# Performance work log

Hardware: AMD Instinct MI355X
Metric: run time of the kernel (lower is better)

The kernel has to match this reference:

```python
import jax, jax.numpy as jnp
import numpy as np


def setup_inputs() -> dict:
    key = jax.random.key(0)
    ks = jax.random.split(key, 12)
    T, A, B = 1024, 32, 8
    V, D = 100000, 128
    H1, H2, C = 512, 256, 100
    s = 0.05
    return {
        "diag_idx": jax.random.randint(ks[0], (T, A, B), 0, V),
        "proc_idx": jax.random.randint(ks[1], (T, A, B), 0, V),
        "embedding": jax.random.normal(ks[2], (V, D), jnp.float32) * s,
        "W_ih": jax.random.normal(ks[3], (4 * H1, 2 * D), jnp.float32) * s,
        "W_hh": jax.random.normal(ks[4], (4 * H1, H1), jnp.float32) * s,
        "b_ih": jax.random.normal(ks[5], (4 * H1,), jnp.float32) * s,
        "b_hh": jax.random.normal(ks[6], (4 * H1,), jnp.float32) * s,
        "W1": jax.random.normal(ks[7], (H2, H1), jnp.float32) * s,
        "b1": jax.random.normal(ks[8], (H2,), jnp.float32) * s,
        "W_out": jax.random.normal(ks[9], (C, H2), jnp.float32) * s,
        "b_out": jax.random.normal(ks[10], (C,), jnp.float32) * s,
    }


def _pool(embedding, idx):
    # idx: [T, A, B] -> gather [T, A, B, D]; mean over items (B), sum over sets (A)
    e = embedding[idx]
    return e.mean(axis=2).sum(axis=1)  # [T, D]


def _lstm(x, W_ih, W_hh, b_ih, b_hh):
    # x: [T, 2D]; PyTorch gate order: i, f, g, o
    H = W_hh.shape[1]
    gx = x @ W_ih.T + (b_ih + b_hh)  # [T, 4H]

    def step(carry, gx_t):
        h, c = carry
        gates = gx_t + h @ W_hh.T
        i, f, g, o = jnp.split(gates, 4)
        i, f, o = jax.nn.sigmoid(i), jax.nn.sigmoid(f), jax.nn.sigmoid(o)
        g = jnp.tanh(g)
        c = f * c + i * g
        h = o * jnp.tanh(c)
        return (h, c), h

    h0 = jnp.zeros((H,), x.dtype)
    c0 = jnp.zeros((H,), x.dtype)
    _, hs = jax.lax.scan(step, (h0, c0), gx)
    return hs  # [T, H]


def reference(diag_idx, proc_idx, embedding, W_ih, W_hh, b_ih, b_hh, W1, b1, W_out, b_out):
    d_vec = _pool(embedding, diag_idx)   # [T, D]
    p_vec = _pool(embedding, proc_idx)   # [T, D]
    x = jnp.concatenate([d_vec, p_vec], axis=-1)  # [T, 2D]
    hs = _lstm(x, W_ih, W_hh, b_ih, b_hh)         # [T, H1]
    h1 = jax.nn.relu(hs @ W1.T + b1)              # [T, H2]
    return h1 @ W_out.T + b_out                   # [T, n_class]
```

## Files before the change

kernel.cpp:

```cpp
#include <hip/hip_runtime.h>

#define T_STEPS 1024
#define A_SETS 32
#define B_ITEMS 8
#define D_EMB 128
#define H1 512
#define H2 256
#define NCLS 100
#define G4H 2048
#define X_DIM 256

#define OFF_X    0
#define OFF_GX   (OFF_X + T_STEPS * X_DIM)
#define OFF_HS   (OFF_GX + T_STEPS * G4H)
#define OFF_SLOT (OFF_HS + T_STEPS * H1)

#define LSTM_G 16

__global__ void init_kernel(float* __restrict__ ws) {
    int tid = threadIdx.x;
    ws[OFF_SLOT + tid] = 0.f;
    ws[OFF_SLOT + 1024 + tid] = 0.f;
}

__global__ void pool_kernel(const int* __restrict__ diag, const int* __restrict__ proc,
                            const float* __restrict__ emb, float* __restrict__ ws) {
    __shared__ int sidx[2][A_SETS * B_ITEMS];
    int t = blockIdx.x;
    int tid = threadIdx.x;
    sidx[0][tid] = diag[t * 256 + tid];
    sidx[1][tid] = proc[t * 256 + tid];
    __syncthreads();
    int src = tid >> 7;
    int d = tid & 127;
    float acc = 0.f;
#pragma unroll 8
    for (int i = 0; i < 256; ++i) {
        acc += emb[(size_t)sidx[src][i] * D_EMB + d];
    }
    ws[OFF_X + t * X_DIM + src * D_EMB + d] = acc * 0.125f;
}

#define GX_TB 8
__global__ void gx_kernel(const float* __restrict__ W_ih, const float* __restrict__ b_ih,
                          const float* __restrict__ b_hh, float* __restrict__ ws) {
    __shared__ float xs[GX_TB][X_DIM];
    int tb = blockIdx.x;
    int jb = blockIdx.y;
    int tid = threadIdx.x;
    const float* x = ws + OFF_X;
    for (int i = tid; i < GX_TB * X_DIM; i += 256)
        xs[i >> 8][i & 255] = x[(size_t)(tb * GX_TB + (i >> 8)) * X_DIM + (i & 255)];
    __syncthreads();
    int row = jb * 256 + tid;
    float b = b_ih[row] + b_hh[row];
    float acc[GX_TB];
#pragma unroll
    for (int i = 0; i < GX_TB; ++i) acc[i] = b;
    const float4* wr = (const float4*)(W_ih + (size_t)row * X_DIM);
#pragma unroll 4
    for (int k4 = 0; k4 < X_DIM / 4; ++k4) {
        float4 w = wr[k4];
#pragma unroll
        for (int i = 0; i < GX_TB; ++i) {
            acc[i] = fmaf(w.x, xs[i][4 * k4 + 0], acc[i]);
            acc[i] = fmaf(w.y, xs[i][4 * k4 + 1], acc[i]);
            acc[i] = fmaf(w.z, xs[i][4 * k4 + 2], acc[i]);
            acc[i] = fmaf(w.w, xs[i][4 * k4 + 3], acc[i]);
        }
    }
    float* gx = ws + OFF_GX;
#pragma unroll
    for (int i = 0; i < GX_TB; ++i)
        gx[(size_t)(tb * GX_TB + i) * G4H + row] = acc[i];
}

__global__ void __launch_bounds__(512, 1)
lstm_kernel(const float* __restrict__ W_hh, float* __restrict__ ws) {
    __shared__ float h_pad[2][4 * 136];
    const int g = blockIdx.x;
    const int tid = threadIdx.x;
    const int lane = tid & 63;
    const int j = tid >> 4;
    const int seg = (tid >> 2) & 3;
    const int gate = tid & 3;
    const int unit = g * 32 + j;
    const int grow = gate * H1 + unit;

    float w[128];
    {
        const float4* wr = (const float4*)(W_hh + (size_t)grow * H1 + seg * 128);
#pragma unroll
        for (int k = 0; k < 32; ++k) {
            float4 v = wr[k];
            w[4 * k + 0] = v.x; w[4 * k + 1] = v.y;
            w[4 * k + 2] = v.z; w[4 * k + 3] = v.w;
        }
    }

    unsigned long long* slots = (unsigned long long*)(ws + OFF_SLOT);
    float* hs = ws + OFF_HS;
    const float* gx = ws + OFF_GX;
    const int stage_row = tid >> 7;
    const int stage_col = tid & 127;
    const bool comb = ((tid & 15) == 0);
    const int base = lane & 48;
    float c = 0.f;

    for (int s = 1; s <= T_STEPS; ++s) {
        const int t = s - 1;
        float gxv = gx[(size_t)t * G4H + grow];
        const unsigned need = (unsigned)(s - 1);
        unsigned long long v;
        do {
            v = __hip_atomic_load(&slots[((s - 1) & 1) * H1 + tid],
                                  __ATOMIC_RELAXED, __HIP_MEMORY_SCOPE_AGENT);
        } while ((unsigned)(v >> 32) < need);
        float* hp = h_pad[s & 1];
        hp[stage_row * 136 + stage_col] = __uint_as_float((unsigned)v);
        __syncthreads();
        float acc = 0.f;
        const float4* h4 = (const float4*)(hp + seg * 136);
#pragma unroll
        for (int k = 0; k < 32; ++k) {
            float4 hv = h4[k];
            acc = fmaf(w[4 * k + 0], hv.x, acc);
            acc = fmaf(w[4 * k + 1], hv.y, acc);
            acc = fmaf(w[4 * k + 2], hv.z, acc);
            acc = fmaf(w[4 * k + 3], hv.w, acc);
        }
        acc += __shfl_xor(acc, 4);
        acc += __shfl_xor(acc, 8);
        acc += gxv;
        float gi = __shfl(acc, base + 0);
        float gf = __shfl(acc, base + 1);
        float gg = __shfl(acc, base + 2);
        float go = __shfl(acc, base + 3);
        if (comb) {
            gi = 1.f / (1.f + __expf(-gi));
            gf = 1.f / (1.f + __expf(-gf));
            go = 1.f / (1.f + __expf(-go));
            gg = tanhf(gg);
            c = fmaf(gf, c, gi * gg);
            float h = go * tanhf(c);
            unsigned long long pv =
                ((unsigned long long)(unsigned)s << 32) | (unsigned long long)__float_as_uint(h);
            __hip_atomic_store(&slots[(s & 1) * H1 + unit], pv,
                               __ATOMIC_RELAXED, __HIP_MEMORY_SCOPE_AGENT);
            hs[(size_t)t * H1 + unit] = h;
        }
    }
}

__global__ void mlp_kernel(const float* __restrict__ W1, const float* __restrict__ b1,
                           const float* __restrict__ W_out, const float* __restrict__ b_out,
                           const float* __restrict__ ws, float* __restrict__ out) {
    __shared__ float hsv[H1];
    __shared__ float h1v[H2];
    int t = blockIdx.x;
    int tid = threadIdx.x;
    const float* hs = ws + OFF_HS;
    hsv[tid] = hs[(size_t)t * H1 + tid];
    hsv[256 + tid] = hs[(size_t)t * H1 + 256 + tid];
    __syncthreads();
    float acc = b1[tid];
    const float4* wr = (const float4*)(W1 + (size_t)tid * H1);
#pragma unroll 4
    for (int k = 0; k < H1 / 4; ++k) {
        float4 w = wr[k];
        acc = fmaf(w.x, hsv[4 * k + 0], acc);
        acc = fmaf(w.y, hsv[4 * k + 1], acc);
        acc = fmaf(w.z, hsv[4 * k + 2], acc);
        acc = fmaf(w.w, hsv[4 * k + 3], acc);
    }
    h1v[tid] = fmaxf(acc, 0.f);
    __syncthreads();
    if (tid < NCLS) {
        float a2 = b_out[tid];
        const float4* w2 = (const float4*)(W_out + (size_t)tid * H2);
#pragma unroll 4
        for (int k = 0; k < H2 / 4; ++k) {
            float4 w = w2[k];
            a2 = fmaf(w.x, h1v[4 * k + 0], a2);
            a2 = fmaf(w.y, h1v[4 * k + 1], a2);
            a2 = fmaf(w.z, h1v[4 * k + 2], a2);
            a2 = fmaf(w.w, h1v[4 * k + 3], a2);
        }
        out[(size_t)t * NCLS + tid] = a2;
    }
}

extern "C" void kernel_launch(void* const* d_in, const int* in_sizes, int n_in,
                              void* d_out, int out_size, void* d_ws, size_t ws_size,
                              hipStream_t stream) {
    const int* diag = (const int*)d_in[0];
    const int* proc = (const int*)d_in[1];
    const float* emb = (const float*)d_in[2];
    const float* W_ih = (const float*)d_in[3];
    const float* W_hh = (const float*)d_in[4];
    const float* b_ih = (const float*)d_in[5];
    const float* b_hh = (const float*)d_in[6];
    const float* W1 = (const float*)d_in[7];
    const float* b1 = (const float*)d_in[8];
    const float* W_out = (const float*)d_in[9];
    const float* b_out = (const float*)d_in[10];
    float* ws = (float*)d_ws;
    float* out = (float*)d_out;

    hipLaunchKernelGGL(init_kernel, dim3(1), dim3(1024), 0, stream, ws);
    hipLaunchKernelGGL(pool_kernel, dim3(T_STEPS), dim3(256), 0, stream, diag, proc, emb, ws);
    hipLaunchKernelGGL(gx_kernel, dim3(T_STEPS / GX_TB, G4H / 256), dim3(256), 0, stream,
                       W_ih, b_ih, b_hh, ws);
    hipLaunchKernelGGL(lstm_kernel, dim3(LSTM_G), dim3(512), 0, stream, W_hh, ws);
    hipLaunchKernelGGL(mlp_kernel, dim3(T_STEPS), dim3(256), 0, stream,
                       W1, b1, W_out, b_out, ws, out);
}
```

Measured before the change: 2.870 ms.

## Spread LSTM recurrence over 32 blocks, use fast gate math, batch MLP timesteps

The persistent LSTM kernel now runs on 32 blocks with 16 hidden units each. Each thread holds 64 weights instead of 128, which cuts per-step FMA chain length and register pressure, at the cost of an extra shuffle reduction and more blocks joining the global spin-wait handshake. The sigmoid and tanh are rewritten with exp plus a hardware reciprocal refined by one Newton step, shortening the serial per-step critical path with slightly different rounding. The MLP kernel processes 8 timesteps per block, so each W1/W_out row load is reused across them, with fewer blocks in exchange.

```diff
diff --git a/kernel.cpp b/kernel.cpp
--- a/kernel.cpp
+++ b/kernel.cpp
@@ -15,7 +15,18 @@
 #define OFF_HS   (OFF_GX + T_STEPS * G4H)
 #define OFF_SLOT (OFF_HS + T_STEPS * H1)
 
-#define LSTM_G 16
+#define LSTM_G 32
+
+__device__ __forceinline__ float fast_rcp(float d) {
+    float r = __builtin_amdgcn_rcpf(d);
+    return r * (2.f - d * r);
+}
+__device__ __forceinline__ float fast_sigmoid(float x) {
+    return fast_rcp(1.f + __expf(-x));
+}
+__device__ __forceinline__ float fast_tanh(float x) {
+    return 1.f - 2.f * fast_rcp(1.f + __expf(2.f * x));
+}
 
 __global__ void init_kernel(float* __restrict__ ws) {
     int tid = threadIdx.x;
@@ -75,36 +86,31 @@
         gx[(size_t)(tb * GX_TB + i) * G4H + row] = acc[i];
 }
 
-__global__ void __launch_bounds__(512, 1)
+__global__ void __launch_bounds__(512, 2)
 lstm_kernel(const float* __restrict__ W_hh, float* __restrict__ ws) {
-    __shared__ float h_pad[2][4 * 136];
+    __shared__ float h_pad[2][8 * 68];
     const int g = blockIdx.x;
     const int tid = threadIdx.x;
     const int lane = tid & 63;
-    const int j = tid >> 4;
-    const int seg = (tid >> 2) & 3;
+    const int j = tid >> 5;
+    const int seg = (tid >> 2) & 7;
     const int gate = tid & 3;
-    const int unit = g * 32 + j;
+    const int unit = g * 16 + j;
     const int grow = gate * H1 + unit;
 
-    float w[128];
+    float4 w4[16];
     {
-        const float4* wr = (const float4*)(W_hh + (size_t)grow * H1 + seg * 128);
-#pragma unroll
-        for (int k = 0; k < 32; ++k) {
-            float4 v = wr[k];
-            w[4 * k + 0] = v.x; w[4 * k + 1] = v.y;
-            w[4 * k + 2] = v.z; w[4 * k + 3] = v.w;
-        }
+        const float4* wr = (const float4*)(W_hh + (size_t)grow * H1 + seg * 64);
+#pragma unroll
+        for (int k = 0; k < 16; ++k) w4[k] = wr[k];
     }
 
     unsigned long long* slots = (unsigned long long*)(ws + OFF_SLOT);
     float* hs = ws + OFF_HS;
     const float* gx = ws + OFF_GX;
-    const int stage_row = tid >> 7;
-    const int stage_col = tid & 127;
-    const bool comb = ((tid & 15) == 0);
-    const int base = lane & 48;
+    const int stage_off = (tid >> 6) * 68 + (tid & 63);
+    const bool comb = ((tid & 31) == 0);
+    const int base = lane & 32;
     float c = 0.f;
 
     for (int s = 1; s <= T_STEPS; ++s) {
@@ -117,32 +123,33 @@
                                   __ATOMIC_RELAXED, __HIP_MEMORY_SCOPE_AGENT);
         } while ((unsigned)(v >> 32) < need);
         float* hp = h_pad[s & 1];
-        hp[stage_row * 136 + stage_col] = __uint_as_float((unsigned)v);
+        hp[stage_off] = __uint_as_float((unsigned)v);
         __syncthreads();
         float acc = 0.f;
-        const float4* h4 = (const float4*)(hp + seg * 136);
-#pragma unroll
-        for (int k = 0; k < 32; ++k) {
+        const float4* h4 = (const float4*)(hp + seg * 68);
+#pragma unroll
+        for (int k = 0; k < 16; ++k) {
             float4 hv = h4[k];
-            acc = fmaf(w[4 * k + 0], hv.x, acc);
-            acc = fmaf(w[4 * k + 1], hv.y, acc);
-            acc = fmaf(w[4 * k + 2], hv.z, acc);
-            acc = fmaf(w[4 * k + 3], hv.w, acc);
+            acc = fmaf(w4[k].x, hv.x, acc);
+            acc = fmaf(w4[k].y, hv.y, acc);
+            acc = fmaf(w4[k].z, hv.z, acc);
+            acc = fmaf(w4[k].w, hv.w, acc);
         }
         acc += __shfl_xor(acc, 4);
         acc += __shfl_xor(acc, 8);
+        acc += __shfl_xor(acc, 16);
         acc += gxv;
         float gi = __shfl(acc, base + 0);
         float gf = __shfl(acc, base + 1);
         float gg = __shfl(acc, base + 2);
         float go = __shfl(acc, base + 3);
         if (comb) {
-            gi = 1.f / (1.f + __expf(-gi));
-            gf = 1.f / (1.f + __expf(-gf));
-            go = 1.f / (1.f + __expf(-go));
-            gg = tanhf(gg);
+            gi = fast_sigmoid(gi);
+            gf = fast_sigmoid(gf);
+            go = fast_sigmoid(go);
+            gg = fast_tanh(gg);
             c = fmaf(gf, c, gi * gg);
-            float h = go * tanhf(c);
+            float h = go * fast_tanh(c);
             unsigned long long pv =
                 ((unsigned long long)(unsigned)s << 32) | (unsigned long long)__float_as_uint(h);
             __hip_atomic_store(&slots[(s & 1) * H1 + unit], pv,
@@ -152,41 +159,53 @@
     }
 }
 
+#define MLP_TB 8
 __global__ void mlp_kernel(const float* __restrict__ W1, const float* __restrict__ b1,
                            const float* __restrict__ W_out, const float* __restrict__ b_out,
                            const float* __restrict__ ws, float* __restrict__ out) {
-    __shared__ float hsv[H1];
-    __shared__ float h1v[H2];
-    int t = blockIdx.x;
+    __shared__ float hsv[MLP_TB][H1];
+    __shared__ float h1v[MLP_TB][H2];
+    int t0 = blockIdx.x * MLP_TB;
     int tid = threadIdx.x;
     const float* hs = ws + OFF_HS;
-    hsv[tid] = hs[(size_t)t * H1 + tid];
-    hsv[256 + tid] = hs[(size_t)t * H1 + 256 + tid];
-    __syncthreads();
-    float acc = b1[tid];
+    for (int i = tid; i < MLP_TB * H1; i += 256)
+        hsv[i >> 9][i & 511] = hs[(size_t)t0 * H1 + i];
+    __syncthreads();
+    float b = b1[tid];
+    float acc[MLP_TB];
+#pragma unroll
+    for (int i = 0; i < MLP_TB; ++i) acc[i] = b;
     const float4* wr = (const float4*)(W1 + (size_t)tid * H1);
 #pragma unroll 4
     for (int k = 0; k < H1 / 4; ++k) {
         float4 w = wr[k];
-        acc = fmaf(w.x, hsv[4 * k + 0], acc);
-        acc = fmaf(w.y, hsv[4 * k + 1], acc);
-        acc = fmaf(w.z, hsv[4 * k + 2], acc);
-        acc = fmaf(w.w, hsv[4 * k + 3], acc);
-    }
-    h1v[tid] = fmaxf(acc, 0.f);
+#pragma unroll
+        for (int i = 0; i < MLP_TB; ++i) {
+            acc[i] = fmaf(w.x, hsv[i][4 * k + 0], acc[i]);
+            acc[i] = fmaf(w.y, hsv[i][4 * k + 1], acc[i]);
+            acc[i] = fmaf(w.z, hsv[i][4 * k + 2], acc[i]);
+            acc[i] = fmaf(w.w, hsv[i][4 * k + 3], acc[i]);
+        }
+    }
+#pragma unroll
+    for (int i = 0; i < MLP_TB; ++i) h1v[i][tid] = fmaxf(acc[i], 0.f);
     __syncthreads();
     if (tid < NCLS) {
-        float a2 = b_out[tid];
         const float4* w2 = (const float4*)(W_out + (size_t)tid * H2);
+        float b2 = b_out[tid];
+#pragma unroll
+        for (int i = 0; i < MLP_TB; ++i) {
+            float a2 = b2;
 #pragma unroll 4
-        for (int k = 0; k < H2 / 4; ++k) {
-            float4 w = w2[k];
-            a2 = fmaf(w.x, h1v[4 * k + 0], a2);
-            a2 = fmaf(w.y, h1v[4 * k + 1], a2);
-            a2 = fmaf(w.z, h1v[4 * k + 2], a2);
-            a2 = fmaf(w.w, h1v[4 * k + 3], a2);
-        }
-        out[(size_t)t * NCLS + tid] = a2;
+            for (int k = 0; k < H2 / 4; ++k) {
+                float4 w = w2[k];
+                a2 = fmaf(w.x, h1v[i][4 * k + 0], a2);
+                a2 = fmaf(w.y, h1v[i][4 * k + 1], a2);
+                a2 = fmaf(w.z, h1v[i][4 * k + 2], a2);
+                a2 = fmaf(w.w, h1v[i][4 * k + 3], a2);
+            }
+            out[(size_t)(t0 + i) * NCLS + tid] = a2;
+        }
     }
 }
 
@@ -212,6 +231,6 @@
     hipLaunchKernelGGL(gx_kernel, dim3(T_STEPS / GX_TB, G4H / 256), dim3(256), 0, stream,
                        W_ih, b_ih, b_hh, ws);
     hipLaunchKernelGGL(lstm_kernel, dim3(LSTM_G), dim3(512), 0, stream, W_hh, ws);
-    hipLaunchKernelGGL(mlp_kernel, dim3(T_STEPS), dim3(256), 0, stream,
+    hipLaunchKernelGGL(mlp_kernel, dim3(T_STEPS / MLP_TB), dim3(256), 0, stream,
                        W1, b1, W_out, b_out, ws, out);
 }
```

Result: faster. 2.699 ms (-6.0%).
